# Performance work log

Measured on AMD Instinct MI355X. Metric: run time of the kernel, lower is better.

Reference implementation:

```python
import jax, jax.numpy as jnp
import numpy as np

N_EMBD = 384
N_HEADS = 6
HEAD_SIZE = N_EMBD // N_HEADS  # 64
D_FF = 4 * N_EMBD
EPS = 1e-5


def layernorm(x, g, b):
    mu = jnp.mean(x, axis=-1, keepdims=True)
    var = jnp.var(x, axis=-1, keepdims=True)
    return (x - mu) * jax.lax.rsqrt(var + EPS) * g + b


def setup_inputs() -> dict:
    key = jax.random.key(0)
    ks = jax.random.split(key, 12)
    B, T, C, H, HS = 64, 256, N_EMBD, N_HEADS, HEAD_SIZE
    s = 0.02
    return {
        "x": jax.random.normal(ks[0], (B, T, C), jnp.float32),
        "Wq": jax.random.normal(ks[1], (H, C, HS), jnp.float32) * s,
        "Wk": jax.random.normal(ks[2], (H, C, HS), jnp.float32) * s,
        "Wv": jax.random.normal(ks[3], (H, C, HS), jnp.float32) * s,
        "Wo": jax.random.normal(ks[4], (C, C), jnp.float32) * s,
        "bo": jnp.zeros((C,), jnp.float32),
        "W1": jax.random.normal(ks[5], (C, D_FF), jnp.float32) * s,
        "b1": jnp.zeros((D_FF,), jnp.float32),
        "W2": jax.random.normal(ks[6], (D_FF, C), jnp.float32) * s,
        "b2": jnp.zeros((C,), jnp.float32),
        "g1": jnp.ones((C,), jnp.float32),
        "beta1": jnp.zeros((C,), jnp.float32),
        "g2": jnp.ones((C,), jnp.float32),
        "beta2": jnp.zeros((C,), jnp.float32),
    }


def reference(x, Wq, Wk, Wv, Wo, bo, W1, b1, W2, b2, g1, beta1, g2, beta2):
    B, T, C = x.shape
    # --- attention branch (dropout = identity in eval) ---
    h = layernorm(x, g1, beta1)
    q = jnp.einsum('btc,hck->bhtk', h, Wq)
    k = jnp.einsum('btc,hck->bhtk', h, Wk)
    v = jnp.einsum('btc,hck->bhtk', h, Wv)
    scale = HEAD_SIZE ** -0.5
    wei = jnp.einsum('bhtk,bhsk->bhts', q, k) * scale  # [B,H,T,T]
    causal = jnp.tril(jnp.ones((T, T), bool))
    wei = jnp.where(causal, wei, -jnp.inf)
    wei = jax.nn.softmax(wei, axis=-1)
    attn = jnp.einsum('bhts,bhsk->bthk', wei, v).reshape(B, T, C)
    x = x + attn @ Wo + bo
    # --- MLP branch ---
    h2 = layernorm(x, g2, beta2)
    ff = jax.nn.relu(h2 @ W1 + b1) @ W2 + b2
    return x + ff
```

## Files before the change

### kernel.cpp

```cpp
#include <hip/hip_runtime.h>

#define B 64
#define T 256
#define C 384
#define H 6
#define HS 64
#define DFF 1536
#define BT (B*T)

typedef __attribute__((ext_vector_type(8))) short short8;
typedef __attribute__((ext_vector_type(4))) float float4v;
typedef __attribute__((ext_vector_type(4))) unsigned short ushort4v;

static __device__ __forceinline__ unsigned short f2bf(float f) {
  unsigned int u = __float_as_uint(f);
  unsigned int r = (u + 0x7fffu + ((u >> 16) & 1u)) >> 16;
  return (unsigned short)r;
}

typedef __attribute__((address_space(1))) const unsigned int ga_u32;
typedef __attribute__((address_space(3))) unsigned int ls_u32;
static __device__ __forceinline__ void gld16(const void* g, void* l) {
  __builtin_amdgcn_global_load_lds((ga_u32*)g, (ls_u32*)l, 16, 0, 0);
}

__global__ __launch_bounds__(256) void prep_w(
    const float* __restrict__ Wq, const float* __restrict__ Wk, const float* __restrict__ Wv,
    const float* __restrict__ Wo, const float* __restrict__ W1, const float* __restrict__ W2,
    unsigned short* __restrict__ wqkv, unsigned short* __restrict__ wo,
    unsigned short* __restrict__ w1t, unsigned short* __restrict__ w2t) {
  __shared__ float tile[32][33];
  int bx = blockIdx.x;
  int x = threadIdx.x & 31, y = threadIdx.x >> 5;
  if (bx < 432) {
    int tn = bx % 36, tc = bx / 36;
    int n0 = tn * 32, c0 = tc * 32;
    int mat = n0 / 384, rem = n0 % 384, head = rem / 64, hs0 = rem % 64;
    const float* W = (mat == 0) ? Wq : ((mat == 1) ? Wk : Wv);
    const float* src = W + (size_t)head * C * HS + hs0;
    #pragma unroll
    for (int i = 0; i < 4; ++i) tile[y + 8 * i][x] = src[(size_t)(c0 + y + 8 * i) * 64 + x];
    __syncthreads();
    #pragma unroll
    for (int i = 0; i < 4; ++i)
      wqkv[(size_t)(n0 + y + 8 * i) * 384 + c0 + x] = f2bf(tile[x][y + 8 * i]);
    return;
  }
  const float* src; unsigned short* dst; int CN, R, n0, c0;
  if (bx < 576) {
    int t = bx - 432; n0 = (t % 12) * 32; c0 = (t / 12) * 32;
    src = Wo; dst = wo; CN = 384; R = 384;
  } else if (bx < 1152) {
    int t = bx - 576; n0 = (t % 48) * 32; c0 = (t / 48) * 32;
    src = W1; dst = w1t; CN = 1536; R = 384;
  } else {
    int t = bx - 1152; n0 = (t % 12) * 32; c0 = (t / 12) * 32;
    src = W2; dst = w2t; CN = 384; R = 1536;
  }
  #pragma unroll
  for (int i = 0; i < 4; ++i) tile[y + 8 * i][x] = src[(size_t)(c0 + y + 8 * i) * CN + n0 + x];
  __syncthreads();
  #pragma unroll
  for (int i = 0; i < 4; ++i)
    dst[(size_t)(n0 + y + 8 * i) * R + c0 + x] = f2bf(tile[x][y + 8 * i]);
}

__global__ __launch_bounds__(256) void ln_kernel(const float* __restrict__ x,
    const float* __restrict__ g, const float* __restrict__ bta,
    unsigned short* __restrict__ out) {
  int t = blockIdx.x * 4 + (threadIdx.x >> 6);
  int lane = threadIdx.x & 63;
  const float* row = x + (size_t)t * C;
  float v[6];
  float s = 0.f, ss = 0.f;
  #pragma unroll
  for (int i = 0; i < 6; ++i) {
    v[i] = row[lane + i * 64];
    s += v[i];
    ss += v[i] * v[i];
  }
  #pragma unroll
  for (int m = 32; m >= 1; m >>= 1) {
    s += __shfl_xor(s, m);
    ss += __shfl_xor(ss, m);
  }
  float mu = s / C;
  float var = ss / C - mu * mu;
  float rstd = rsqrtf(var + 1e-5f);
  unsigned short* orow = out + (size_t)t * C;
  #pragma unroll
  for (int i = 0; i < 6; ++i) {
    int c = lane + i * 64;
    orow[c] = f2bf((v[i] - mu) * rstd * g[c] + bta[c]);
  }
}

template<int EPI, int MT>
__global__ __launch_bounds__(MT >= 256 ? 512 : 256) void gemm_kernel(
    const unsigned short* __restrict__ A, const unsigned short* __restrict__ Wt,
    const float* __restrict__ bias, const float* __restrict__ resid,
    float* __restrict__ outf,
    unsigned short* __restrict__ outb, unsigned short* __restrict__ outb2,
    unsigned short* __restrict__ outb3, int K, int N) {
  __shared__ unsigned short Ash[MT * 64];
  __shared__ unsigned short Bsh[128 * 64];
  constexpr int NW = (MT >= 256) ? 8 : 4;
  constexpr int WM = NW / 2;
  constexpr int MR = MT / WM / 16;
  constexpr int NA = (MT / 8) / NW;
  constexpr int NB = 16 / NW;
  int tid = threadIdx.x, lane = tid & 63, w = tid >> 6;
  int wm = w >> 1, wn = w & 1;
  int bxs = ((blockIdx.x & 7) * (gridDim.x >> 3)) + (blockIdx.x >> 3);
  int m0 = bxs * MT, n0 = blockIdx.y * 128;
  int lrow = lane >> 3;
  int lchunk = (lane & 7) ^ (lrow & 7);
  int frow = lane & 15, cg = lane >> 4;
  float4v acc[MR][4] = {};
  for (int k0 = 0; k0 < K; k0 += 64) {
    __syncthreads();
    #pragma unroll
    for (int i = 0; i < NA; ++i) {
      int win = w * NA + i;
      gld16(A + (size_t)(m0 + win * 8 + lrow) * K + k0 + lchunk * 8, &Ash[win * 512]);
    }
    #pragma unroll
    for (int i = 0; i < NB; ++i) {
      int win = w * NB + i;
      gld16(Wt + (size_t)(n0 + win * 8 + lrow) * K + k0 + lchunk * 8, &Bsh[win * 512]);
    }
    __syncthreads();
    #pragma unroll
    for (int ks = 0; ks < 2; ++ks) {
      short8 af[MR], bf[4];
      #pragma unroll
      for (int mi = 0; mi < MR; ++mi) {
        int r = wm * (MR * 16) + mi * 16 + frow;
        int ch = (ks * 4 + cg) ^ (r & 7);
        af[mi] = *(const short8*)((const char*)Ash + r * 128 + ch * 16);
      }
      #pragma unroll
      for (int ni = 0; ni < 4; ++ni) {
        int r = wn * 64 + ni * 16 + frow;
        int ch = (ks * 4 + cg) ^ (r & 7);
        bf[ni] = *(const short8*)((const char*)Bsh + r * 128 + ch * 16);
      }
      #pragma unroll
      for (int mi = 0; mi < MR; ++mi)
        #pragma unroll
        for (int ni = 0; ni < 4; ++ni)
          acc[mi][ni] = __builtin_amdgcn_mfma_f32_16x16x32_bf16(af[mi], bf[ni], acc[mi][ni], 0, 0, 0);
    }
  }
  int cl = lane & 15;
  #pragma unroll
  for (int mi = 0; mi < MR; ++mi) {
    #pragma unroll
    for (int ni = 0; ni < 4; ++ni) {
      if constexpr (EPI == 0) {
        int gc = n0 + wn * 64 + ni * 16 + cl;
        int mat = gc / 384;
        int head = (gc % 384) >> 6;
        int hs = gc & 63;
        int gr0 = m0 + wm * (MR * 16) + mi * 16 + cg * 4;
        int tt0 = gr0 & 255, bidx = gr0 >> 8;
        size_t bhb = (size_t)(bidx * H + head);
        if (mat == 2) {
          ushort4v pk;
          #pragma unroll
          for (int j = 0; j < 4; ++j) pk[j] = f2bf(acc[mi][ni][j]);
          *(ushort4v*)&outb3[(bhb * HS + hs) * T + tt0] = pk;
        } else {
          unsigned short* dst = (mat == 0) ? outb : outb2;
          #pragma unroll
          for (int j = 0; j < 4; ++j)
            dst[(bhb * T + tt0 + j) * HS + hs] = f2bf(acc[mi][ni][j]);
        }
      } else {
        #pragma unroll
        for (int j = 0; j < 4; ++j) {
          int gr = m0 + wm * (MR * 16) + mi * 16 + cg * 4 + j;
          int gc = n0 + wn * 64 + ni * 16 + cl;
          float val = acc[mi][ni][j];
          if constexpr (EPI == 2) {
            outb[(size_t)gr * N + gc] = f2bf(fmaxf(val + bias[gc], 0.f));
          } else {
            size_t i = (size_t)gr * N + gc;
            outf[i] = resid[i] + val + bias[gc];
          }
        }
      }
    }
  }
}

__global__ __launch_bounds__(512) void proj_ln_kernel(
    const unsigned short* __restrict__ A, const unsigned short* __restrict__ Wt,
    const float* __restrict__ bo, const float* __restrict__ x,
    const float* __restrict__ g2, const float* __restrict__ be2,
    float* __restrict__ x2, unsigned short* __restrict__ h2) {
  __shared__ unsigned short Ash[32 * 64];
  __shared__ unsigned short Bsh[384 * 64];
  __shared__ float red[32][4][2];
  int tid = threadIdx.x, lane = tid & 63, w = tid >> 6;
  int wm = w >> 2, wn = w & 3;
  int bxs = ((blockIdx.x & 7) * (gridDim.x >> 3)) + (blockIdx.x >> 3);
  int m0 = bxs * 32;
  int lrow = lane >> 3;
  int lchunk = (lane & 7) ^ (lrow & 7);
  int frow = lane & 15, cg = lane >> 4, cl = lane & 15;
  float4v acc[6] = {};
  for (int k0 = 0; k0 < 384; k0 += 64) {
    __syncthreads();
    if (w < 4) gld16(A + (size_t)(m0 + w * 8 + lrow) * 384 + k0 + lchunk * 8, &Ash[w * 512]);
    #pragma unroll
    for (int i = 0; i < 6; ++i) {
      int win = w * 6 + i;
      gld16(Wt + (size_t)(win * 8 + lrow) * 384 + k0 + lchunk * 8, &Bsh[win * 512]);
    }
    __syncthreads();
    #pragma unroll
    for (int ks = 0; ks < 2; ++ks) {
      int ra = wm * 16 + frow;
      int cha = (ks * 4 + cg) ^ (ra & 7);
      short8 af = *(const short8*)((const char*)Ash + ra * 128 + cha * 16);
      #pragma unroll
      for (int nt = 0; nt < 6; ++nt) {
        int rb = wn * 96 + nt * 16 + frow;
        int chb = (ks * 4 + cg) ^ (rb & 7);
        short8 bf = *(const short8*)((const char*)Bsh + rb * 128 + chb * 16);
        acc[nt] = __builtin_amdgcn_mfma_f32_16x16x32_bf16(af, bf, acc[nt], 0, 0, 0);
      }
    }
  }
  #pragma unroll
  for (int nt = 0; nt < 6; ++nt) {
    int gc = wn * 96 + nt * 16 + cl;
    #pragma unroll
    for (int j = 0; j < 4; ++j) {
      int gr = m0 + wm * 16 + cg * 4 + j;
      acc[nt][j] += x[(size_t)gr * 384 + gc] + bo[gc];
    }
  }
  __syncthreads();
  #pragma unroll
  for (int j = 0; j < 4; ++j) {
    float s = 0.f, ss = 0.f;
    #pragma unroll
    for (int nt = 0; nt < 6; ++nt) { float v = acc[nt][j]; s += v; ss += v * v; }
    #pragma unroll
    for (int off = 1; off < 16; off <<= 1) { s += __shfl_xor(s, off); ss += __shfl_xor(ss, off); }
    if (cl == 0) {
      int lr = wm * 16 + cg * 4 + j;
      red[lr][wn][0] = s;
      red[lr][wn][1] = ss;
    }
  }
  __syncthreads();
  #pragma unroll
  for (int j = 0; j < 4; ++j) {
    int lr = wm * 16 + cg * 4 + j;
    int gr = m0 + lr;
    float s = red[lr][0][0] + red[lr][1][0] + red[lr][2][0] + red[lr][3][0];
    float ss = red[lr][0][1] + red[lr][1][1] + red[lr][2][1] + red[lr][3][1];
    float mu = s / 384.f;
    float var = ss / 384.f - mu * mu;
    float rstd = rsqrtf(var + 1e-5f);
    #pragma unroll
    for (int nt = 0; nt < 6; ++nt) {
      int gc = wn * 96 + nt * 16 + cl;
      float v = acc[nt][j];
      x2[(size_t)gr * 384 + gc] = v;
      h2[(size_t)gr * 384 + gc] = f2bf((v - mu) * rstd * g2[gc] + be2[gc]);
    }
  }
}

__global__ __launch_bounds__(256) void attn_kernel(
    const unsigned short* __restrict__ qg, const unsigned short* __restrict__ kg,
    const unsigned short* __restrict__ vtg, unsigned short* __restrict__ ab) {
  __shared__ unsigned short Ksh[64 * 64];
  __shared__ unsigned short Vsh[64 * 256];
  __shared__ unsigned short Psh[4 * 16 * 256];
  int bh = blockIdx.x;
  int bb = bh / H, hh = bh % H;
  int qt = blockIdx.y, q0 = qt * 64;
  int tid = threadIdx.x, lane = tid & 63, w = tid >> 6;
  int cl = lane & 15, cg = lane >> 4;
  const float scale_log2e = 0.125f * 1.44269504f;
  const unsigned short* qp = qg + ((size_t)bh * T) * HS;
  const unsigned short* kp = kg + ((size_t)bh * T) * HS;
  const unsigned short* vp = vtg + ((size_t)bh * HS) * T;

  short8 aq[2];
  #pragma unroll
  for (int k0 = 0; k0 < 2; ++k0)
    aq[k0] = *(const short8*)&qp[(size_t)(q0 + w * 16 + cl) * HS + cg * 8 + k0 * 32];

  #pragma unroll
  for (int i = 0; i < 8; ++i) {
    int idx = tid + i * 256;
    int r = idx >> 5, c16 = idx & 31;
    uint4 val = *(const uint4*)&vp[(size_t)r * T + c16 * 8];
    int byte = (r * 512 + c16 * 16) ^ ((r & 7) << 4);
    *(uint4*)((char*)Vsh + byte) = val;
  }

  float4v sacc[4][4] = {};
  for (int si = 0; si <= qt; ++si) {
    __syncthreads();
    #pragma unroll
    for (int i = 0; i < 2; ++i) {
      int idx = tid + i * 256;
      int r = idx >> 3, c16 = idx & 7;
      uint4 val = *(const uint4*)&kp[(size_t)(si * 64 + r) * HS + c16 * 8];
      int byte = (r * 128 + c16 * 16) ^ ((r & 7) << 4);
      *(uint4*)((char*)Ksh + byte) = val;
    }
    __syncthreads();
    #pragma unroll
    for (int ss = 0; ss < 4; ++ss) {
      if (ss == si) {
        #pragma unroll
        for (int nt = 0; nt < 4; ++nt) {
          int srow = nt * 16 + cl;
          #pragma unroll
          for (int k0 = 0; k0 < 2; ++k0) {
            int byte = (srow * 128 + (cg * 8 + k0 * 32) * 2) ^ ((srow & 7) << 4);
            short8 bf = *(const short8*)((char*)Ksh + byte);
            sacc[ss][nt] = __builtin_amdgcn_mfma_f32_16x16x32_bf16(aq[k0], bf, sacc[ss][nt], 0, 0, 0);
          }
        }
      }
    }
  }

  #pragma unroll
  for (int si = 0; si < 4; ++si) {
    if (si == qt) {
      #pragma unroll
      for (int nt = 0; nt < 4; ++nt) {
        int s = q0 + nt * 16 + cl;
        #pragma unroll
        for (int j = 0; j < 4; ++j) {
          int q = q0 + w * 16 + cg * 4 + j;
          if (s > q) sacc[si][nt][j] = -1e30f;
        }
      }
    }
  }

  float lj[4];
  #pragma unroll
  for (int j = 0; j < 4; ++j) {
    float m = -1e30f;
    #pragma unroll
    for (int si = 0; si < 4; ++si) if (si <= qt)
      #pragma unroll
      for (int nt = 0; nt < 4; ++nt) m = fmaxf(m, sacc[si][nt][j]);
    #pragma unroll
    for (int off = 1; off < 16; off <<= 1) m = fmaxf(m, __shfl_xor(m, off));
    float l = 0.f;
    #pragma unroll
    for (int si = 0; si < 4; ++si) if (si <= qt)
      #pragma unroll
      for (int nt = 0; nt < 4; ++nt) {
        float p0 = exp2f((sacc[si][nt][j] - m) * scale_log2e);
        sacc[si][nt][j] = p0;
        l += p0;
      }
    #pragma unroll
    for (int off = 1; off < 16; off <<= 1) l += __shfl_xor(l, off);
    lj[j] = 1.f / l;
  }

  char* pbase = (char*)Psh + w * 8192;
  #pragma unroll
  for (int si = 0; si < 4; ++si) if (si <= qt)
    #pragma unroll
    for (int nt = 0; nt < 4; ++nt)
      #pragma unroll
      for (int j = 0; j < 4; ++j) {
        int prow = cg * 4 + j, col = si * 64 + nt * 16 + cl;
        int byte = (prow * 512 + col * 2) ^ ((prow & 7) << 4);
        *(unsigned short*)(pbase + byte) = f2bf(sacc[si][nt][j]);
      }

  int nks = 2 * (qt + 1);
  #pragma unroll
  for (int nt = 0; nt < 4; ++nt) {
    float4v oacc = {};
    for (int ks = 0; ks < nks; ++ks) {
      int k = ks * 32 + cg * 8;
      int pbyte = (cl * 512 + k * 2) ^ ((cl & 7) << 4);
      short8 af = *(const short8*)(pbase + pbyte);
      int vr = nt * 16 + cl;
      int vbyte = (vr * 512 + k * 2) ^ ((vr & 7) << 4);
      short8 bf = *(const short8*)((char*)Vsh + vbyte);
      oacc = __builtin_amdgcn_mfma_f32_16x16x32_bf16(af, bf, oacc, 0, 0, 0);
    }
    #pragma unroll
    for (int j = 0; j < 4; ++j) {
      int t = q0 + w * 16 + cg * 4 + j;
      ab[((size_t)(bb * T + t)) * C + hh * 64 + nt * 16 + cl] = f2bf(oacc[j] * lj[j]);
    }
  }
}

extern "C" void kernel_launch(void* const* d_in, const int* in_sizes, int n_in,
                              void* d_out, int out_size, void* d_ws, size_t ws_size,
                              hipStream_t stream) {
  const float* x   = (const float*)d_in[0];
  const float* Wq  = (const float*)d_in[1];
  const float* Wk  = (const float*)d_in[2];
  const float* Wv  = (const float*)d_in[3];
  const float* Wo  = (const float*)d_in[4];
  const float* bo  = (const float*)d_in[5];
  const float* W1  = (const float*)d_in[6];
  const float* b1  = (const float*)d_in[7];
  const float* W2  = (const float*)d_in[8];
  const float* b2  = (const float*)d_in[9];
  const float* g1  = (const float*)d_in[10];
  const float* be1 = (const float*)d_in[11];
  const float* g2  = (const float*)d_in[12];
  const float* be2 = (const float*)d_in[13];
  float* out = (float*)d_out;
  float* ws = (float*)d_ws;

  unsigned short* wqkv_t = (unsigned short*)ws;
  unsigned short* wo_t   = wqkv_t + 442368;
  unsigned short* w1t    = wo_t + 147456;
  unsigned short* w2t    = w1t + 589824;
  float* base2 = ws + 884736;
  unsigned short* h  = (unsigned short*)base2;
  float* x2 = base2 + 3145728;
  unsigned short* ab = (unsigned short*)(x2 + 6291456);
  unsigned short* qb = (unsigned short*)(x2 + 6291456 + 3145728);
  unsigned short* kb = qb + 6291456;
  unsigned short* vt = kb + 6291456;
  unsigned short* ffb = ab;

  prep_w<<<1728, 256, 0, stream>>>(Wq, Wk, Wv, Wo, W1, W2, wqkv_t, wo_t, w1t, w2t);
  ln_kernel<<<BT / 4, 256, 0, stream>>>(x, g1, be1, h);
  gemm_kernel<0, 256><<<dim3(64, 9), 512, 0, stream>>>(h, wqkv_t, nullptr, nullptr,
                                                       nullptr, qb, kb, vt, 384, 1152);
  attn_kernel<<<dim3(B * H, T / 64), 256, 0, stream>>>(qb, kb, vt, ab);
  proj_ln_kernel<<<512, 512, 0, stream>>>(ab, wo_t, bo, x, g2, be2, x2, h);
  gemm_kernel<2, 256><<<dim3(64, 12), 512, 0, stream>>>(h, w1t, b1, nullptr,
                                                        nullptr, ffb, nullptr, nullptr, 384, 1536);
  gemm_kernel<3, 64><<<dim3(256, 3), 256, 0, stream>>>(ffb, w2t, b2, x2,
                                                       out, nullptr, nullptr, nullptr, 1536, 384);
}
```

Before: 149.4 us.

## Shrink GEMM tiles for more blocks and store residual stream in bf16

Generalizes the GEMM kernel to take an N-tile size and switches all GEMMs to 256-thread blocks with smaller tiles (128x64, 64x64), doubling grid sizes for better CU occupancy and load balance. Separately, the intermediate residual x2 is stored as bf16 instead of fp32, halving that write and read traffic. The smaller tiles lower per-block data reuse, and the bf16 residual loses precision in the output path.

```diff
diff --git a/kernel.cpp b/kernel.cpp
--- a/kernel.cpp
+++ b/kernel.cpp
@@ -16,6 +16,9 @@
   unsigned int u = __float_as_uint(f);
   unsigned int r = (u + 0x7fffu + ((u >> 16) & 1u)) >> 16;
   return (unsigned short)r;
+}
+static __device__ __forceinline__ float bf2f(unsigned short s) {
+  return __uint_as_float((unsigned int)s << 16);
 }
 
 typedef __attribute__((address_space(1))) const unsigned int ga_u32;
@@ -95,28 +98,27 @@
   }
 }
 
-template<int EPI, int MT>
-__global__ __launch_bounds__(MT >= 256 ? 512 : 256) void gemm_kernel(
+template<int EPI, int MT, int NT>
+__global__ __launch_bounds__(256) void gemm_kernel(
     const unsigned short* __restrict__ A, const unsigned short* __restrict__ Wt,
-    const float* __restrict__ bias, const float* __restrict__ resid,
+    const float* __restrict__ bias, const unsigned short* __restrict__ residb,
     float* __restrict__ outf,
     unsigned short* __restrict__ outb, unsigned short* __restrict__ outb2,
     unsigned short* __restrict__ outb3, int K, int N) {
   __shared__ unsigned short Ash[MT * 64];
-  __shared__ unsigned short Bsh[128 * 64];
-  constexpr int NW = (MT >= 256) ? 8 : 4;
-  constexpr int WM = NW / 2;
-  constexpr int MR = MT / WM / 16;
-  constexpr int NA = (MT / 8) / NW;
-  constexpr int NB = 16 / NW;
+  __shared__ unsigned short Bsh[NT * 64];
+  constexpr int MR = MT / 32;
+  constexpr int NR = NT / 32;
+  constexpr int NA = MT / 32;
+  constexpr int NB = NT / 32;
   int tid = threadIdx.x, lane = tid & 63, w = tid >> 6;
   int wm = w >> 1, wn = w & 1;
   int bxs = ((blockIdx.x & 7) * (gridDim.x >> 3)) + (blockIdx.x >> 3);
-  int m0 = bxs * MT, n0 = blockIdx.y * 128;
+  int m0 = bxs * MT, n0 = blockIdx.y * NT;
   int lrow = lane >> 3;
   int lchunk = (lane & 7) ^ (lrow & 7);
   int frow = lane & 15, cg = lane >> 4;
-  float4v acc[MR][4] = {};
+  float4v acc[MR][NR] = {};
   for (int k0 = 0; k0 < K; k0 += 64) {
     __syncthreads();
     #pragma unroll
@@ -132,7 +134,7 @@
     __syncthreads();
     #pragma unroll
     for (int ks = 0; ks < 2; ++ks) {
-      short8 af[MR], bf[4];
+      short8 af[MR], bf[NR];
       #pragma unroll
       for (int mi = 0; mi < MR; ++mi) {
         int r = wm * (MR * 16) + mi * 16 + frow;
@@ -140,15 +142,15 @@
         af[mi] = *(const short8*)((const char*)Ash + r * 128 + ch * 16);
       }
       #pragma unroll
-      for (int ni = 0; ni < 4; ++ni) {
-        int r = wn * 64 + ni * 16 + frow;
+      for (int ni = 0; ni < NR; ++ni) {
+        int r = wn * (NR * 16) + ni * 16 + frow;
         int ch = (ks * 4 + cg) ^ (r & 7);
         bf[ni] = *(const short8*)((const char*)Bsh + r * 128 + ch * 16);
       }
       #pragma unroll
       for (int mi = 0; mi < MR; ++mi)
         #pragma unroll
-        for (int ni = 0; ni < 4; ++ni)
+        for (int ni = 0; ni < NR; ++ni)
           acc[mi][ni] = __builtin_amdgcn_mfma_f32_16x16x32_bf16(af[mi], bf[ni], acc[mi][ni], 0, 0, 0);
     }
   }
@@ -156,9 +158,9 @@
   #pragma unroll
   for (int mi = 0; mi < MR; ++mi) {
     #pragma unroll
-    for (int ni = 0; ni < 4; ++ni) {
+    for (int ni = 0; ni < NR; ++ni) {
       if constexpr (EPI == 0) {
-        int gc = n0 + wn * 64 + ni * 16 + cl;
+        int gc = n0 + wn * (NR * 16) + ni * 16 + cl;
         int mat = gc / 384;
         int head = (gc % 384) >> 6;
         int hs = gc & 63;
@@ -180,13 +182,13 @@
         #pragma unroll
         for (int j = 0; j < 4; ++j) {
           int gr = m0 + wm * (MR * 16) + mi * 16 + cg * 4 + j;
-          int gc = n0 + wn * 64 + ni * 16 + cl;
+          int gc = n0 + wn * (NR * 16) + ni * 16 + cl;
           float val = acc[mi][ni][j];
           if constexpr (EPI == 2) {
             outb[(size_t)gr * N + gc] = f2bf(fmaxf(val + bias[gc], 0.f));
           } else {
             size_t i = (size_t)gr * N + gc;
-            outf[i] = resid[i] + val + bias[gc];
+            outf[i] = bf2f(residb[i]) + val + bias[gc];
           }
         }
       }
@@ -198,7 +200,7 @@
     const unsigned short* __restrict__ A, const unsigned short* __restrict__ Wt,
     const float* __restrict__ bo, const float* __restrict__ x,
     const float* __restrict__ g2, const float* __restrict__ be2,
-    float* __restrict__ x2, unsigned short* __restrict__ h2) {
+    unsigned short* __restrict__ x2b, unsigned short* __restrict__ h2) {
   __shared__ unsigned short Ash[32 * 64];
   __shared__ unsigned short Bsh[384 * 64];
   __shared__ float red[32][4][2];
@@ -270,7 +272,7 @@
     for (int nt = 0; nt < 6; ++nt) {
       int gc = wn * 96 + nt * 16 + cl;
       float v = acc[nt][j];
-      x2[(size_t)gr * 384 + gc] = v;
+      x2b[(size_t)gr * 384 + gc] = f2bf(v);
       h2[(size_t)gr * 384 + gc] = f2bf((v - mu) * rstd * g2[gc] + be2[gc]);
     }
   }
@@ -433,21 +435,21 @@
   unsigned short* w2t    = w1t + 589824;
   float* base2 = ws + 884736;
   unsigned short* h  = (unsigned short*)base2;
-  float* x2 = base2 + 3145728;
-  unsigned short* ab = (unsigned short*)(x2 + 6291456);
-  unsigned short* qb = (unsigned short*)(x2 + 6291456 + 3145728);
+  unsigned short* x2b = (unsigned short*)(base2 + 3145728);
+  unsigned short* ab = (unsigned short*)(base2 + 3145728 + 6291456);
+  unsigned short* qb = ab + 6291456;
   unsigned short* kb = qb + 6291456;
   unsigned short* vt = kb + 6291456;
   unsigned short* ffb = ab;
 
   prep_w<<<1728, 256, 0, stream>>>(Wq, Wk, Wv, Wo, W1, W2, wqkv_t, wo_t, w1t, w2t);
   ln_kernel<<<BT / 4, 256, 0, stream>>>(x, g1, be1, h);
-  gemm_kernel<0, 256><<<dim3(64, 9), 512, 0, stream>>>(h, wqkv_t, nullptr, nullptr,
-                                                       nullptr, qb, kb, vt, 384, 1152);
+  gemm_kernel<0, 128, 64><<<dim3(128, 18), 256, 0, stream>>>(h, wqkv_t, nullptr, nullptr,
+                                                             nullptr, qb, kb, vt, 384, 1152);
   attn_kernel<<<dim3(B * H, T / 64), 256, 0, stream>>>(qb, kb, vt, ab);
-  proj_ln_kernel<<<512, 512, 0, stream>>>(ab, wo_t, bo, x, g2, be2, x2, h);
-  gemm_kernel<2, 256><<<dim3(64, 12), 512, 0, stream>>>(h, w1t, b1, nullptr,
-                                                        nullptr, ffb, nullptr, nullptr, 384, 1536);
-  gemm_kernel<3, 64><<<dim3(256, 3), 256, 0, stream>>>(ffb, w2t, b2, x2,
-                                                       out, nullptr, nullptr, nullptr, 1536, 384);
-}
+  proj_ln_kernel<<<512, 512, 0, stream>>>(ab, wo_t, bo, x, g2, be2, x2b, h);
+  gemm_kernel<2, 128, 64><<<dim3(128, 24), 256, 0, stream>>>(h, w1t, b1, nullptr,
+                                                             nullptr, ffb, nullptr, nullptr, 384, 1536);
+  gemm_kernel<3, 64, 64><<<dim3(256, 6), 256, 0, stream>>>(ffb, w2t, b2, x2b,
+                                                           out, nullptr, nullptr, nullptr, 1536, 384);
+}
```

Measured after the change: 150.7 us. Within noise of the previous version (+0.9%).
